# Kernel tuning notes

Hardware: AMD Instinct MI355X
Metric: run time of the kernel (lower is better)

The kernel has to match this reference:

```python
import jax, jax.numpy as jnp
import numpy as np

S = 1024   # speakers_per_batch
U = 64     # utterances_per_speaker
E = 256    # model_embedding_size


def setup_inputs() -> dict:
    key = jax.random.key(0)
    k1, _ = jax.random.split(key)
    # embeds as produced by forward(): relu'd then L2-normalized rows
    raw = jax.nn.relu(jax.random.normal(k1, (S * U, E), dtype=jnp.float32))
    embeds = raw / (jnp.linalg.norm(raw, axis=1, keepdims=True) + 1e-12)
    return {
        "embeds": embeds,
        "similarity_weight": jnp.array([10.0], dtype=jnp.float32),
        "similarity_bias": jnp.array([-5.0], dtype=jnp.float32),
    }


def reference(embeds, similarity_weight, similarity_bias):
    e = embeds.reshape(S, U, E)                      # [S,U,E]
    # inclusive centroids (per speaker)
    c_incl = jnp.mean(e, axis=1)                     # [S,E]
    incl_norm = jnp.linalg.norm(c_incl, axis=1)      # [S]
    # exclusive centroids (leave-one-out per utterance)
    c_excl = (jnp.sum(e, axis=1, keepdims=True) - e) / (U - 1)  # [S,U,E]
    excl_norm = jnp.linalg.norm(c_excl, axis=2)      # [S,U]
    # off-diagonal (k != j): cosine vs inclusive centroid of speaker k
    sim = jnp.einsum('jue,ke->juk', e, c_incl) / incl_norm       # [S,U,S]
    # diagonal (k == j): cosine vs own exclusive centroid
    diag = jnp.einsum('jue,jue->ju', e, c_excl) / excl_norm      # [S,U]
    idx = jnp.arange(S)
    sim = sim.at[idx, :, idx].set(diag)
    sim = sim * similarity_weight[0] + similarity_bias[0]
    # cross-entropy against ground truth speaker ids
    logits = sim.reshape(S * U, S)                   # [SU,S]
    gt = jnp.repeat(jnp.arange(S), U)                # [SU]
    logp = jax.nn.log_softmax(logits, axis=-1)
    loss = -jnp.mean(jnp.take_along_axis(logp, gt[:, None], axis=1))
    preds = jnp.argmax(logits, axis=1)
    accuracy = jnp.mean((preds == gt).astype(jnp.float32))
    return loss, accuracy
```

## Files before the change

kernel.cpp:

```cpp
#include <hip/hip_runtime.h>
#include <math.h>

#define NS 1024
#define NU 64
#define NE 256

typedef __attribute__((ext_vector_type(4))) float f32x4;
typedef long i64x2 __attribute__((ext_vector_type(2)));

__device__ static inline unsigned int pk4_fp8(float a, float b, float c,
                                              float d) {
  int r = 0;
  r = __builtin_amdgcn_cvt_pk_fp8_f32(a, b, r, false);
  r = __builtin_amdgcn_cvt_pk_fp8_f32(c, d, r, true);
  return (unsigned int)r;
}


__global__ __launch_bounds__(256) void centroid_kernel(
    const float* __restrict__ embeds, unsigned int* __restrict__ Cb,
    unsigned long long* __restrict__ Ab, float* __restrict__ normsum,
    float* __restrict__ ssumG, unsigned int* __restrict__ pmaxG,
    float* __restrict__ out) {
  int k = blockIdx.x;
  int t = threadIdx.x;
  if (t < 64) {
    ssumG[k * 64 + t] = 0.f;
    pmaxG[k * 64 + t] = 0u;
  }
  int wave = t >> 6, e4 = t & 63;

  const float4* base =
      (const float4*)(embeds + (size_t)k * NU * NE) + wave * 16 * 64 + e4;
  float4 s = {0.f, 0.f, 0.f, 0.f};
#pragma unroll
  for (int i = 0; i < 16; ++i) {
    float4 v = base[i * 64];
    s.x += v.x; s.y += v.y; s.z += v.z; s.w += v.w;
  }
  __shared__ float4 ps[4][64];
  ps[wave][e4] = s;
  __syncthreads();
  if (t < 64) {
    float4 a = ps[0][t], b = ps[1][t], c = ps[2][t], d = ps[3][t];
    float4 s4;
    s4.x = a.x + b.x + c.x + d.x;
    s4.y = a.y + b.y + c.y + d.y;
    s4.z = a.z + b.z + c.z + d.z;
    s4.w = a.w + b.w + c.w + d.w;
    float sq = s4.x * s4.x + s4.y * s4.y + s4.z * s4.z + s4.w * s4.w;
#pragma unroll
    for (int off = 32; off; off >>= 1) sq += __shfl_xor(sq, off, 64);
    float nrm = sqrtf(sq);
    float inv = 1.f / nrm;
    unsigned int v = pk4_fp8(s4.x * inv, s4.y * inv, s4.z * inv, s4.w * inv);
    int lane_ = (((t >> 1) & 3) * 16 + (k & 15));
    int idx = (k >> 4) * 1024 + (t >> 4) * 256 + lane_ * 4 +
              (((t >> 3) & 1) << 1) + (t & 1);
    Cb[idx] = v;
    if (t == 0) {
      normsum[k] = nrm;
      if (k == 0) { out[0] = 0.f; out[1] = 0.f; }
    }
  }

  {
    int tile = t >> 6;
    int l = t & 63;
    int m = l & 15, qq = l >> 4;
    const float* rowp = embeds + (size_t)(k * 64 + tile * 16 + m) * NE;
    i64x2* Ab2 = (i64x2*)Ab;
    size_t base2 = ((size_t)k * 4 + tile) * 256 + l;
#pragma unroll
    for (int s2 = 0; s2 < 4; ++s2) {
      unsigned long long u[2];
#pragma unroll
      for (int half = 0; half < 2; ++half) {
        int sI = 2 * s2 + half;
        int k0 = sI * 32 + qq * 8;
        float4 x = *(const float4*)(rowp + k0);
        float4 y = *(const float4*)(rowp + k0 + 4);
        unsigned int lo = pk4_fp8(x.x, x.y, x.z, x.w);
        unsigned int hi = pk4_fp8(y.x, y.y, y.z, y.w);
        u[half] = ((unsigned long long)hi << 32) | lo;
      }
      i64x2 v;
      v.x = (long)u[0];
      v.y = (long)u[1];
      Ab2[base2 + s2 * 64] = v;
    }
  }
}

__global__ __launch_bounds__(256) void main_kernel(
    const long* __restrict__ Ab, const long* __restrict__ Cb,
    const float* __restrict__ normsum, const float* __restrict__ wp,
    const float* __restrict__ bp, float* __restrict__ ssumG,
    unsigned int* __restrict__ pmaxG, float* __restrict__ pdiagG) {
  int t = threadIdx.x;
  int wave = t >> 6, lane = t & 63;
  int c = lane & 15, q = lane >> 4;
  int b = blockIdx.x;
  int rg = b >> 1;
  int h = b & 1;
  int jspk = rg;
  int r0 = rg * 64 + wave * 16;

  float w = *wp, bia = *bp;
  const float L2E = 1.4426950408889634f;
  float M0 = fabsf(w) + bia;
  float wl = w * L2E;
  float cl = (bia - M0) * L2E;
  float ns = normsum[jspk];

  const i64x2* Av = (const i64x2*)Ab;
  const i64x2* Bv = (const i64x2*)Cb;

  long af[8];
  {
    int ab2 = (rg * 4 + wave) * 256 + lane;
#pragma unroll
    for (int s2 = 0; s2 < 4; ++s2) {
      i64x2 v = Av[ab2 + s2 * 64];
      af[2 * s2] = v.x;
      af[2 * s2 + 1] = v.y;
    }
  }

  float ssum[4], pm[4];
#pragma unroll
  for (int r = 0; r < 4; ++r) {
    ssum[r] = 0.f;
    pm[r] = 0.f;
  }

  auto prefetch = [&](i64x2 (&BF)[4], int Tt) {
    int cb = (h * 32 + Tt) * 256 + lane;
#pragma unroll
    for (int s2 = 0; s2 < 4; ++s2) BF[s2] = Bv[cb + s2 * 64];
  };

  auto tile = [&](f32x4& ACC, const i64x2 (&BF)[4]) {
    ACC = (f32x4){0.f, 0.f, 0.f, 0.f};
    __builtin_amdgcn_s_setprio(1);
#pragma unroll
    for (int s2 = 0; s2 < 4; ++s2) {
      ACC = __builtin_amdgcn_mfma_f32_16x16x32_fp8_fp8(af[2 * s2], BF[s2].x,
                                                       ACC, 0, 0, 0);
      ACC = __builtin_amdgcn_mfma_f32_16x16x32_fp8_fp8(af[2 * s2 + 1],
                                                       BF[s2].y, ACC, 0, 0, 0);
    }
    __builtin_amdgcn_s_setprio(0);
  };

  auto epilogue = [&](f32x4& ACC, int Tt) {
    int gt = h * 32 + Tt;
    bool diagstep = ((jspk >> 4) == gt);
    f32x4 a = ACC;
    if (diagstep && c == (jspk & 15)) {
#pragma unroll
      for (int r = 0; r < 4; ++r) {
        float Sv = a[r] * ns;
        float den = fmaxf(fmaf(ns, ns, 1.f) - 2.f * Sv, 1e-30f);
        float val = (Sv - 1.f) * __frsqrt_rn(den);
        float pd = exp2f(fmaf(val, wl, cl));
        pdiagG[r0 + q * 4 + r] = pd;
        a[r] = val;
      }
    }
#pragma unroll
    for (int r = 0; r < 4; ++r) {
      float p = exp2f(fmaf(a[r], wl, cl));
      ssum[r] += p;
      pm[r] = fmaxf(pm[r], p);
    }
  };

  i64x2 bf0[4], bf1[4];
  f32x4 accA, accB;
  prefetch(bf0, 0);
  prefetch(bf1, 1);
  tile(accA, bf0);
#pragma unroll 1
  for (int T = 1; T < 31; T += 2) {
    prefetch(bf0, T + 1);
    tile(accB, bf1);
    epilogue(accA, T - 1);
    prefetch(bf1, T + 2);
    tile(accA, bf0);
    epilogue(accB, T);
  }
  tile(accB, bf1);
  epilogue(accA, 30);
  epilogue(accB, 31);

#pragma unroll
  for (int r = 0; r < 4; ++r) {
    float s = ssum[r];
    s += __shfl_xor(s, 1, 64);
    s += __shfl_xor(s, 2, 64);
    s += __shfl_xor(s, 4, 64);
    s += __shfl_xor(s, 8, 64);
    float m = pm[r];
    m = fmaxf(m, __shfl_xor(m, 1, 64));
    m = fmaxf(m, __shfl_xor(m, 2, 64));
    m = fmaxf(m, __shfl_xor(m, 4, 64));
    m = fmaxf(m, __shfl_xor(m, 8, 64));
    if (c == 0) {
      int row = r0 + q * 4 + r;
      atomicAdd(&ssumG[row], s);
      atomicMax(&pmaxG[row], __float_as_uint(m));
    }
  }
}

__global__ __launch_bounds__(256) void reduce_kernel(
    const float* __restrict__ ssumG, const unsigned int* __restrict__ pmaxG,
    const float* __restrict__ pdiagG, float* __restrict__ out) {
  int i = blockIdx.x * 256 + threadIdx.x;
  float pd = pdiagG[i];
  float lossr = __logf(ssumG[i] / pd);
  float corr = (pd >= __uint_as_float(pmaxG[i])) ? 1.f : 0.f;
#pragma unroll
  for (int off = 32; off; off >>= 1) {
    lossr += __shfl_xor(lossr, off, 64);
    corr += __shfl_xor(corr, off, 64);
  }
  __shared__ float pl[4], pc[4];
  int wave = threadIdx.x >> 6, lane = threadIdx.x & 63;
  if (lane == 0) { pl[wave] = lossr; pc[wave] = corr; }
  __syncthreads();
  if (threadIdx.x == 0) {
    const float inv = 1.f / (float)(NS * NU);
    atomicAdd(&out[0], (pl[0] + pl[1] + pl[2] + pl[3]) * inv);
    atomicAdd(&out[1], (pc[0] + pc[1] + pc[2] + pc[3]) * inv);
  }
}

extern "C" void kernel_launch(void* const* d_in, const int* in_sizes, int n_in,
                              void* d_out, int out_size, void* d_ws,
                              size_t ws_size, hipStream_t stream) {
  const float* embeds = (const float*)d_in[0];
  const float* w = (const float*)d_in[1];
  const float* b = (const float*)d_in[2];
  float* out = (float*)d_out;
  char* ws = (char*)d_ws;
  unsigned int* Cb = (unsigned int*)ws;
  unsigned int* pmaxG = (unsigned int*)(ws + (256 << 10));
  float* ssumG = (float*)(ws + (512 << 10));
  float* pdiagG = (float*)(ws + (768 << 10));
  float* normsum = (float*)(ws + (1024 << 10));
  unsigned long long* Ab =
      (unsigned long long*)(ws + (1056 << 10));

  centroid_kernel<<<NS, 256, 0, stream>>>(embeds, Cb, Ab, normsum, ssumG,
                                          pmaxG, out);
  main_kernel<<<2048, 256, 0, stream>>>((const long*)Ab, (const long*)Cb,
                                        normsum, w, b, ssumG, pmaxG, pdiagG);
  reduce_kernel<<<NS * NU / 256, 256, 0, stream>>>(ssumG, pmaxG, pdiagG, out);
}
```

Measured before the change: 150.0 us.

## Switch main GEMM to 32x32x16 FP8 MFMA tiles with repacked operand layouts

Repacks the FP8 centroid and embedding buffers for the 32x32x16 MFMA instruction and rewrites the main kernel so each wave computes 32x32 output tiles. The grid is halved to 1024 blocks, and B-operand loads are interleaved inside the tile computation. Softmax exp uses the raw hardware exp2 builtin. The aim is higher MFMA throughput per instruction and fewer tile iterations and reduction shuffles. The cost is more registers (16 accumulators, 16 A fragments, two accumulator sets) and lower occupancy.

```diff
diff --git a/kernel.cpp b/kernel.cpp
--- a/kernel.cpp
+++ b/kernel.cpp
@@ -6,6 +6,7 @@
 #define NE 256
 
 typedef __attribute__((ext_vector_type(4))) float f32x4;
+typedef __attribute__((ext_vector_type(16))) float f32x16;
 typedef long i64x2 __attribute__((ext_vector_type(2)));
 
 __device__ static inline unsigned int pk4_fp8(float a, float b, float c,
@@ -54,9 +55,9 @@
     float nrm = sqrtf(sq);
     float inv = 1.f / nrm;
     unsigned int v = pk4_fp8(s4.x * inv, s4.y * inv, s4.z * inv, s4.w * inv);
-    int lane_ = (((t >> 1) & 3) * 16 + (k & 15));
-    int idx = (k >> 4) * 1024 + (t >> 4) * 256 + lane_ * 4 +
-              (((t >> 3) & 1) << 1) + (t & 1);
+    int lane_ = (k & 31) + 32 * ((t >> 1) & 1);
+    int idx = (k >> 5) * 2048 + (t >> 3) * 256 + lane_ * 4 +
+              (((t >> 2) & 1) << 1) + (t & 1);
     Cb[idx] = v;
     if (t == 0) {
       normsum[k] = nrm;
@@ -65,19 +66,22 @@
   }
 
   {
-    int tile = t >> 6;
+    int tt = t >> 7;
     int l = t & 63;
-    int m = l & 15, qq = l >> 4;
-    const float* rowp = embeds + (size_t)(k * 64 + tile * 16 + m) * NE;
+    int hp = (t >> 6) & 1;
+    int row = k * 64 + tt * 32 + (l & 31);
+    int kbase = (l >> 5) * 8;
+    const float* rowp = embeds + (size_t)row * NE;
     i64x2* Ab2 = (i64x2*)Ab;
-    size_t base2 = ((size_t)k * 4 + tile) * 256 + l;
-#pragma unroll
-    for (int s2 = 0; s2 < 4; ++s2) {
+    size_t rt = (size_t)k * 2 + tt;
+#pragma unroll
+    for (int i = 0; i < 4; ++i) {
+      int sp = hp * 4 + i;
       unsigned long long u[2];
 #pragma unroll
       for (int half = 0; half < 2; ++half) {
-        int sI = 2 * s2 + half;
-        int k0 = sI * 32 + qq * 8;
+        int sI = 2 * sp + half;
+        int k0 = sI * 16 + kbase;
         float4 x = *(const float4*)(rowp + k0);
         float4 y = *(const float4*)(rowp + k0 + 4);
         unsigned int lo = pk4_fp8(x.x, x.y, x.z, x.w);
@@ -87,7 +91,7 @@
       i64x2 v;
       v.x = (long)u[0];
       v.y = (long)u[1];
-      Ab2[base2 + s2 * 64] = v;
+      Ab2[(rt * 8 + sp) * 64 + l] = v;
     }
   }
 }
@@ -99,12 +103,12 @@
     unsigned int* __restrict__ pmaxG, float* __restrict__ pdiagG) {
   int t = threadIdx.x;
   int wave = t >> 6, lane = t & 63;
-  int c = lane & 15, q = lane >> 4;
+  int hi = lane >> 5;
   int b = blockIdx.x;
   int rg = b >> 1;
   int h = b & 1;
-  int jspk = rg;
-  int r0 = rg * 64 + wave * 16;
+  int jspk = rg * 2 + (wave >> 1);
+  int r0 = rg * 128 + wave * 32;
 
   float w = *wp, bia = *bp;
   const float L2E = 1.4426950408889634f;
@@ -115,99 +119,116 @@
 
   const i64x2* Av = (const i64x2*)Ab;
   const i64x2* Bv = (const i64x2*)Cb;
-
-  long af[8];
+  int gt_base = h * 16;
+
+  long af[16];
   {
-    int ab2 = (rg * 4 + wave) * 256 + lane;
-#pragma unroll
-    for (int s2 = 0; s2 < 4; ++s2) {
-      i64x2 v = Av[ab2 + s2 * 64];
-      af[2 * s2] = v.x;
-      af[2 * s2 + 1] = v.y;
-    }
-  }
-
-  float ssum[4], pm[4];
-#pragma unroll
-  for (int r = 0; r < 4; ++r) {
-    ssum[r] = 0.f;
-    pm[r] = 0.f;
-  }
-
-  auto prefetch = [&](i64x2 (&BF)[4], int Tt) {
-    int cb = (h * 32 + Tt) * 256 + lane;
-#pragma unroll
-    for (int s2 = 0; s2 < 4; ++s2) BF[s2] = Bv[cb + s2 * 64];
-  };
-
-  auto tile = [&](f32x4& ACC, const i64x2 (&BF)[4]) {
-    ACC = (f32x4){0.f, 0.f, 0.f, 0.f};
-    __builtin_amdgcn_s_setprio(1);
-#pragma unroll
-    for (int s2 = 0; s2 < 4; ++s2) {
-      ACC = __builtin_amdgcn_mfma_f32_16x16x32_fp8_fp8(af[2 * s2], BF[s2].x,
-                                                       ACC, 0, 0, 0);
-      ACC = __builtin_amdgcn_mfma_f32_16x16x32_fp8_fp8(af[2 * s2 + 1],
-                                                       BF[s2].y, ACC, 0, 0, 0);
-    }
-    __builtin_amdgcn_s_setprio(0);
-  };
-
-  auto epilogue = [&](f32x4& ACC, int Tt) {
-    int gt = h * 32 + Tt;
-    bool diagstep = ((jspk >> 4) == gt);
-    f32x4 a = ACC;
-    if (diagstep && c == (jspk & 15)) {
-#pragma unroll
-      for (int r = 0; r < 4; ++r) {
-        float Sv = a[r] * ns;
+    int rt = rg * 4 + wave;
+#pragma unroll
+    for (int sp = 0; sp < 8; ++sp) {
+      i64x2 v = Av[(rt * 8 + sp) * 64 + lane];
+      af[2 * sp] = v.x;
+      af[2 * sp + 1] = v.y;
+    }
+  }
+
+  float ssum[16], pm[16];
+#pragma unroll
+  for (int i = 0; i < 16; ++i) {
+    ssum[i] = 0.f;
+    pm[i] = 0.f;
+  }
+
+  auto loadBA = [&](i64x2 (&BF)[4], int ct) {
+    int cb = (gt_base + ct) * 512 + lane;
+#pragma unroll
+    for (int sp = 0; sp < 4; ++sp) BF[sp] = Bv[cb + sp * 64];
+  };
+  auto loadBB = [&](i64x2 (&BF)[4], int ct) {
+    int cb = (gt_base + ct) * 512 + lane + 256;
+#pragma unroll
+    for (int i = 0; i < 4; ++i) BF[i] = Bv[cb + i * 64];
+  };
+
+  auto tile = [&](f32x16& ACC, i64x2 (&BA)[4], i64x2 (&BB)[4], int nextT) {
+    f32x16 a;
+#pragma unroll
+    for (int i = 0; i < 16; ++i) a[i] = 0.f;
+    int nt = nextT < 16 ? nextT : 15;
+#pragma unroll
+    for (int sp = 0; sp < 4; ++sp) {
+      a = __builtin_amdgcn_mfma_f32_32x32x16_fp8_fp8(af[2 * sp], BA[sp].x, a,
+                                                     0, 0, 0);
+      a = __builtin_amdgcn_mfma_f32_32x32x16_fp8_fp8(af[2 * sp + 1], BA[sp].y,
+                                                     a, 0, 0, 0);
+    }
+    loadBA(BA, nt);
+#pragma unroll
+    for (int sp = 0; sp < 4; ++sp) {
+      a = __builtin_amdgcn_mfma_f32_32x32x16_fp8_fp8(af[8 + 2 * sp], BB[sp].x,
+                                                     a, 0, 0, 0);
+      a = __builtin_amdgcn_mfma_f32_32x32x16_fp8_fp8(af[9 + 2 * sp], BB[sp].y,
+                                                     a, 0, 0, 0);
+    }
+    loadBB(BB, nt);
+    ACC = a;
+  };
+
+  auto epilogue = [&](f32x16& ACC, int T) {
+    int gt = gt_base + T;
+    bool diagstep = ((jspk >> 5) == gt);
+    f32x16 a = ACC;
+    if (diagstep && (lane & 31) == (jspk & 31)) {
+#pragma unroll
+      for (int i = 0; i < 16; ++i) {
+        float Sv = a[i] * ns;
         float den = fmaxf(fmaf(ns, ns, 1.f) - 2.f * Sv, 1e-30f);
         float val = (Sv - 1.f) * __frsqrt_rn(den);
-        float pd = exp2f(fmaf(val, wl, cl));
-        pdiagG[r0 + q * 4 + r] = pd;
-        a[r] = val;
+        float pd = __builtin_amdgcn_exp2f(fmaf(val, wl, cl));
+        pdiagG[r0 + (i & 3) + 8 * (i >> 2) + 4 * hi] = pd;
+        a[i] = val;
       }
     }
 #pragma unroll
-    for (int r = 0; r < 4; ++r) {
-      float p = exp2f(fmaf(a[r], wl, cl));
-      ssum[r] += p;
-      pm[r] = fmaxf(pm[r], p);
-    }
-  };
-
-  i64x2 bf0[4], bf1[4];
-  f32x4 accA, accB;
-  prefetch(bf0, 0);
-  prefetch(bf1, 1);
-  tile(accA, bf0);
+    for (int i = 0; i < 16; ++i) {
+      float p = __builtin_amdgcn_exp2f(fmaf(a[i], wl, cl));
+      ssum[i] += p;
+      pm[i] = fmaxf(pm[i], p);
+    }
+  };
+
+  i64x2 BA[4], BB[4];
+  f32x16 accA, accB;
+  loadBA(BA, 0);
+  loadBB(BB, 0);
+  tile(accA, BA, BB, 1);
 #pragma unroll 1
-  for (int T = 1; T < 31; T += 2) {
-    prefetch(bf0, T + 1);
-    tile(accB, bf1);
+  for (int T = 1; T < 15; T += 2) {
+    tile(accB, BA, BB, T + 1);
     epilogue(accA, T - 1);
-    prefetch(bf1, T + 2);
-    tile(accA, bf0);
+    tile(accA, BA, BB, T + 2);
     epilogue(accB, T);
   }
-  tile(accB, bf1);
-  epilogue(accA, 30);
-  epilogue(accB, 31);
-
-#pragma unroll
-  for (int r = 0; r < 4; ++r) {
-    float s = ssum[r];
+  tile(accB, BA, BB, 16);
+  epilogue(accA, 14);
+  epilogue(accB, 15);
+
+#pragma unroll
+  for (int i = 0; i < 16; ++i) {
+    float s = ssum[i];
     s += __shfl_xor(s, 1, 64);
     s += __shfl_xor(s, 2, 64);
     s += __shfl_xor(s, 4, 64);
     s += __shfl_xor(s, 8, 64);
-    float m = pm[r];
+    s += __shfl_xor(s, 16, 64);
+    float m = pm[i];
     m = fmaxf(m, __shfl_xor(m, 1, 64));
     m = fmaxf(m, __shfl_xor(m, 2, 64));
     m = fmaxf(m, __shfl_xor(m, 4, 64));
     m = fmaxf(m, __shfl_xor(m, 8, 64));
-    if (c == 0) {
-      int row = r0 + q * 4 + r;
+    m = fmaxf(m, __shfl_xor(m, 16, 64));
+    if ((lane & 31) == 0) {
+      int row = r0 + (i & 3) + 8 * (i >> 2) + 4 * hi;
       atomicAdd(&ssumG[row], s);
       atomicMax(&pmaxG[row], __float_as_uint(m));
     }
@@ -255,7 +276,7 @@
 
   centroid_kernel<<<NS, 256, 0, stream>>>(embeds, Cb, Ab, normsum, ssumG,
                                           pmaxG, out);
-  main_kernel<<<2048, 256, 0, stream>>>((const long*)Ab, (const long*)Cb,
+  main_kernel<<<1024, 256, 0, stream>>>((const long*)Ab, (const long*)Cb,
                                         normsum, w, b, ssumG, pmaxG, pdiagG);
   reduce_kernel<<<NS * NU / 256, 256, 0, stream>>>(ssumG, pmaxG, pdiagG, out);
 }
```

Measured after the change: 151.9 us. No clear change (+1.3%).
